# Performance work log

Measured on AMD Instinct MI355X. Metric: run time of the kernel, lower is better.

The kernel has to match this reference:

```python
import jax, jax.numpy as jnp
import numpy as np

HEADS = 4
SCALE = 8.0
LN_EPS = 1e-5
L2_EPS = 1e-12

def _l2norm(t):
    # F.normalize(dim=-1): t / max(||t||_2, eps)
    n = jnp.sqrt(jnp.sum(t * t, axis=-1, keepdims=True))
    return t / jnp.maximum(n, L2_EPS)

def setup_inputs() -> dict:
    key = jax.random.key(0)
    k1, k2, k3 = jax.random.split(key, 3)
    b, c, h, w = 16, 256, 32, 32
    inner = HEADS * 64
    x = jax.random.normal(k1, (b, c, h, w), dtype=jnp.float32)
    g = jnp.ones((1, c, 1, 1), dtype=jnp.float32)
    w_qkv = jax.random.normal(k2, (3 * inner, c), dtype=jnp.float32) * (1.0 / np.sqrt(c))
    w_out = jax.random.normal(k3, (c, inner), dtype=jnp.float32) * (1.0 / np.sqrt(inner))
    return {"x": x, "g": g, "w_qkv": w_qkv, "w_out": w_out}

def reference(x, g, w_qkv, w_out):
    b, c, H, W = x.shape
    n = H * W
    # channel LayerNorm (lucidrains style): mean/var over channel dim, learned gain g
    mean = jnp.mean(x, axis=1, keepdims=True)
    var = jnp.mean((x - mean) ** 2, axis=1, keepdims=True)  # unbiased=False
    xn = (x - mean) * jax.lax.rsqrt(var + LN_EPS) * g
    # 1x1 conv QKV == channel matmul
    qkv = jnp.einsum('bchw,oc->bohw', xn, w_qkv)  # [b, 3*inner, H, W]
    q, k, v = jnp.split(qkv, 3, axis=1)
    def to_bhnd(t):
        d = t.shape[1] // HEADS
        return t.reshape(b, HEADS, d, n).transpose(0, 1, 3, 2)  # b h n d
    q, k, v = map(to_bhnd, (q, k, v))
    q, k = _l2norm(q), _l2norm(k)
    sim = jnp.einsum('bhid,bhjd->bhij', q, k) * SCALE
    attn = jax.nn.softmax(sim, axis=-1)
    out = jnp.einsum('bhij,bhjd->bhid', attn, v)
    out = out.transpose(0, 1, 3, 2).reshape(b, -1, H, W)  # b (h d) H W
    return jnp.einsum('bchw,oc->bohw', out, w_out) + x
```

## Files before the change

kernel.cpp:

```cpp
#include <hip/hip_runtime.h>
#include <hip/hip_bf16.h>

typedef short short4v __attribute__((ext_vector_type(4)));
typedef short short8v __attribute__((ext_vector_type(8)));
typedef float float4v __attribute__((ext_vector_type(4)));
typedef __bf16 bf16x8 __attribute__((ext_vector_type(8)));

typedef __attribute__((address_space(1))) const unsigned int g_uint;
typedef __attribute__((address_space(3))) unsigned int lds_uint;

__device__ __forceinline__ unsigned short f2bf(float f) {
    union { float f; unsigned int i; } t;
    t.f = f;
    unsigned int u = t.i;
    u += 0x7fffu + ((u >> 16) & 1u);
    return (unsigned short)(u >> 16);
}

__device__ __forceinline__ short bfcast(float f) {
    __bf16 h = (__bf16)f;
    return __builtin_bit_cast(short, h);
}

__device__ __forceinline__ float fast_exp2(float x) {
    float r;
    asm("v_exp_f32 %0, %1\n\ts_nop 0" : "=v"(r) : "v"(x));
    return r;
}

__device__ __forceinline__ void gload_lds16(const unsigned short* g, unsigned short* l) {
    __builtin_amdgcn_global_load_lds((g_uint*)g, (lds_uint*)l, 16, 0, 0);
}

__device__ __forceinline__ bf16x8 frag128(const unsigned short* t, int row, int slot) {
    return *reinterpret_cast<const bf16x8*>(
        reinterpret_cast<const char*>(t) + row * 128 + (((slot ^ (row & 7)) << 4)));
}

__device__ __forceinline__ float4v mfma32(bf16x8 a, bf16x8 b, float4v c) {
    return __builtin_amdgcn_mfma_f32_16x16x32_bf16(a, b, c, 0, 0, 0);
}

__global__ __launch_bounds__(256) void prep_kernel(const float* __restrict__ wq,
                                                   const float* __restrict__ wo,
                                                   unsigned short* __restrict__ wqb,
                                                   unsigned short* __restrict__ wob) {
    int i = blockIdx.x * 256 + threadIdx.x;
    if (i < 196608) wqb[i] = f2bf(wq[i]);
    else            wob[i - 196608] = f2bf(wo[i - 196608]);
}

__global__ __launch_bounds__(256) void ln_kernel(const float* __restrict__ x,
                                                 const float* __restrict__ g,
                                                 unsigned short* __restrict__ xnT) {
    __shared__ float red[2][4][64];
    const int tid = threadIdx.x;
    const int p = tid & 63, cg = tid >> 6;
    const int b = blockIdx.y;
    const int pix = blockIdx.x * 64 + p;
    const float* xb = x + ((size_t)b << 18) + pix;

    float v[64];
    float s = 0.f, q = 0.f;
    #pragma unroll
    for (int cc = 0; cc < 64; ++cc) {
        v[cc] = xb[(cg * 64 + cc) << 10];
        s += v[cc]; q += v[cc] * v[cc];
    }
    red[0][cg][p] = s; red[1][cg][p] = q;
    __syncthreads();
    float ts = red[0][0][p] + red[0][1][p] + red[0][2][p] + red[0][3][p];
    float tq = red[1][0][p] + red[1][1][p] + red[1][2][p] + red[1][3][p];
    float mean = ts * (1.f / 256.f);
    float var  = tq * (1.f / 256.f) - mean * mean;
    float rstd = rsqrtf(var + 1e-5f);
    float bias = -mean * rstd;

    unsigned short* dst = xnT + (((size_t)b << 10) + pix) * 256 + cg * 64;
    #pragma unroll
    for (int cc = 0; cc < 64; cc += 8) {
        union { uint4 u; unsigned short s[8]; } pk;
        #pragma unroll
        for (int j = 0; j < 8; ++j)
            pk.s[j] = f2bf(fmaf(v[cc + j], rstd, bias) * g[cg * 64 + cc + j]);
        *reinterpret_cast<uint4*>(dst + cc) = pk.u;
    }
}

__global__ __launch_bounds__(256) void qkv_gemm(const unsigned short* __restrict__ xnT,
                                                const unsigned short* __restrict__ wqkv,
                                                unsigned short* __restrict__ qhat,
                                                unsigned short* __restrict__ khatT,
                                                unsigned short* __restrict__ vperm) {
    __shared__ __align__(16) unsigned short sW[8192];
    __shared__ __align__(16) unsigned short sX[8192];
    const int tid = threadIdx.x, lane = tid & 63, w = tid >> 6;
    const int l16 = lane & 15, g = lane >> 4;
    const int id = blockIdx.x;
    const int xcd = id & 7, sIdx = id >> 3;
    const int m = sIdx % 12, tq = sIdx / 12;
    const int t = xcd + (tq << 3);
    const int pb = t & 15, b = t >> 4;

    const unsigned short* Wbase = wqkv + m * 64 * 256;
    const unsigned short* Xbase = xnT + (((size_t)b << 10) + pb * 64) * 256;

    const int srow = (lane >> 3);
    const int sslot = lane & 7;

    auto stage = [&](int buf, int k0) {
        #pragma unroll
        for (int ii = 0; ii < 2; ++ii) {
            int inst = w + 4 * ii;
            int row = inst * 8 + srow;
            int src = row * 256 + k0 + 8 * (sslot ^ (row & 7));
            gload_lds16(Wbase + src, &sW[buf * 4096 + inst * 512]);
            gload_lds16(Xbase + src, &sX[buf * 4096 + inst * 512]);
        }
    };

    float4v acc[4] = {{0,0,0,0},{0,0,0,0},{0,0,0,0},{0,0,0,0}};
    const bool qk = (m < 8);

    stage(0, 0);
    __syncthreads();
    for (int ks = 0; ks < 4; ++ks) {
        if (ks < 3) stage((ks + 1) & 1, (ks + 1) * 64);
        const unsigned short* Wt = &sW[(ks & 1) * 4096];
        const unsigned short* Xt = &sX[(ks & 1) * 4096];
        #pragma unroll
        for (int kk = 0; kk < 2; ++kk) {
            bf16x8 aF = frag128(qk ? Xt : Wt, 16 * w + l16, 4 * kk + g);
            #pragma unroll
            for (int jt = 0; jt < 4; ++jt) {
                bf16x8 bF = frag128(qk ? Wt : Xt, 16 * jt + l16, 4 * kk + g);
                acc[jt] = mfma32(aF, bF, acc[jt]);
            }
        }
        __syncthreads();
    }

    if (qk) {
        float rn[4];
        #pragma unroll
        for (int r = 0; r < 4; ++r) {
            float s = acc[0][r]*acc[0][r] + acc[1][r]*acc[1][r]
                    + acc[2][r]*acc[2][r] + acc[3][r]*acc[3][r];
            s += __shfl_xor(s, 1, 64);
            s += __shfl_xor(s, 2, 64);
            s += __shfl_xor(s, 4, 64);
            s += __shfl_xor(s, 8, 64);
            rn[r] = rsqrtf(fmaxf(s, 1e-24f));
        }
        int h = m & 3;
        int bh = b * 4 + h;
        if (m < 4) {
            unsigned short* qb = qhat + ((size_t)bh << 16) + (size_t)(pb * 64 + 16 * w) * 64;
            #pragma unroll
            for (int jt = 0; jt < 4; ++jt)
                #pragma unroll
                for (int r = 0; r < 4; ++r)
                    qb[(4 * g + r) * 64 + 16 * jt + l16] =
                        f2bf(acc[jt][r] * (rn[r] * 11.541560327111707f));
        } else {
            unsigned short* kb = khatT + ((size_t)(bh * 16 + pb)) * 4096;
            #pragma unroll
            for (int jt = 0; jt < 4; ++jt)
                #pragma unroll
                for (int r = 0; r < 4; ++r) {
                    int j = 16 * w + 4 * g + r;
                    int d = 16 * jt + l16;
                    kb[j * 64 + (((d >> 3) ^ (j & 7)) << 3) + (d & 7)] =
                        f2bf(acc[jt][r] * rn[r]);
                }
        }
    } else {
        int bh = b * 4 + (m - 8);
        unsigned short* vb = vperm + ((size_t)(bh * 16 + pb)) * 4096;
        #pragma unroll
        for (int jt = 0; jt < 4; ++jt) {
            int cphi = (l16 >> 2) * 2 + (jt >> 1);
            int cplo = (jt & 1) * 4 + (l16 & 3);
            #pragma unroll
            for (int r = 0; r < 4; ++r) {
                int d = 16 * w + 4 * g + r;
                vb[d * 64 + ((cphi ^ (d & 7)) << 3) + cplo] = f2bf(acc[jt][r]);
            }
        }
    }
}

__global__ __launch_bounds__(512, 4) void attn_kernel(const unsigned short* __restrict__ qhat,
                                                      const unsigned short* __restrict__ khatT,
                                                      const unsigned short* __restrict__ vperm,
                                                      unsigned short* __restrict__ oT) {
    __shared__ __align__(16) unsigned short smem[16384];
    const int tid = threadIdx.x, lane = tid & 63, w = tid >> 6;
    const int l16 = lane & 15, g = lane >> 4;
    const int id = blockIdx.x;
    const int sIdx = id >> 3;
    const int bh = (id & 7) * 8 + (sIdx >> 3);
    const int qb = sIdx & 7;
    const int b = bh >> 2, h = bh & 3;

    const unsigned short* Qg = qhat + ((size_t)bh << 16) + (size_t)(qb * 128) * 64;
    const unsigned short* Kt = khatT + ((size_t)(bh * 16)) * 4096;
    const unsigned short* Vt = vperm + ((size_t)(bh * 16)) * 4096;

    bf16x8 bq[2];
    #pragma unroll
    for (int ds = 0; ds < 2; ++ds)
        bq[ds] = *reinterpret_cast<const bf16x8*>(
            Qg + (16 * w + l16) * 64 + 32 * ds + 8 * g);

    auto stage = [&](int buf, int t) {
        unsigned short* kb = &smem[buf * 8192 + w * 512];
        unsigned short* vb = &smem[buf * 8192 + 4096 + w * 512];
        gload_lds16(Kt + t * 4096 + w * 512 + lane * 8, kb);
        gload_lds16(Vt + t * 4096 + w * 512 + lane * 8, vb);
    };

    float lsum = 0.f;
    float4v oacc[4] = {};

    stage(0, 0);
    __syncthreads();

    for (int t = 0; t < 16; ++t) {
        const unsigned short* kb = &smem[(t & 1) * 8192];
        const unsigned short* vb = kb + 4096;
        if (t < 15) stage((t + 1) & 1, t + 1);

        float4v st[4] = {};
        #pragma unroll
        for (int ds = 0; ds < 2; ++ds) {
            bf16x8 ak[4];
            #pragma unroll
            for (int jt = 0; jt < 4; ++jt)
                ak[jt] = frag128(kb, 16 * jt + l16, 4 * ds + g);
            __builtin_amdgcn_s_setprio(1);
            #pragma unroll
            for (int jt = 0; jt < 4; ++jt)
                st[jt] = mfma32(ak[jt], bq[ds], st[jt]);
            __builtin_amdgcn_s_setprio(0);
        }

        short8v vv[4][2];
        #pragma unroll
        for (int dt = 0; dt < 4; ++dt) {
            int row = 16 * dt + l16;
            #pragma unroll
            for (int q = 0; q < 2; ++q)
                vv[dt][q] = *reinterpret_cast<const short8v*>(
                    reinterpret_cast<const char*>(vb) + row * 128 +
                    (((2 * g + q) ^ (row & 7)) << 4));
        }

        short4v pf[4];
        #pragma unroll
        for (int jt = 0; jt < 4; ++jt) {
            float p0 = fast_exp2(st[jt][0]);
            float p1 = fast_exp2(st[jt][1]);
            float p2 = fast_exp2(st[jt][2]);
            float p3 = fast_exp2(st[jt][3]);
            lsum += (p0 + p1) + (p2 + p3);
            short4v tt;
            tt[0] = bfcast(p0); tt[1] = bfcast(p1);
            tt[2] = bfcast(p2); tt[3] = bfcast(p3);
            pf[jt] = tt;
        }

        __builtin_amdgcn_s_setprio(1);
        #pragma unroll
        for (int dt = 0; dt < 4; ++dt)
            #pragma unroll
            for (int q = 0; q < 2; ++q) {
                short4v lo = __builtin_shufflevector(vv[dt][q], vv[dt][q], 0, 1, 2, 3);
                short4v hi = __builtin_shufflevector(vv[dt][q], vv[dt][q], 4, 5, 6, 7);
                oacc[dt] = __builtin_amdgcn_mfma_f32_16x16x16bf16_1k(
                    lo, pf[2 * q], oacc[dt], 0, 0, 0);
                oacc[dt] = __builtin_amdgcn_mfma_f32_16x16x16bf16_1k(
                    hi, pf[2 * q + 1], oacc[dt], 0, 0, 0);
            }
        __builtin_amdgcn_s_setprio(0);

        __syncthreads();
    }

    lsum += __shfl_xor(lsum, 16, 64);
    lsum += __shfl_xor(lsum, 32, 64);
    float inv = 1.f / lsum;

    unsigned short* OL = smem;
    {
        int irow = 16 * w + l16;
        #pragma unroll
        for (int dt = 0; dt < 4; ++dt)
            #pragma unroll
            for (int r = 0; r < 4; ++r)
                OL[irow * 72 + 16 * dt + 4 * g + r] = f2bf(oacc[dt][r] * inv);
    }
    __syncthreads();
    {
        int row = tid >> 2, q4 = tid & 3;
        unsigned short* dst = oT + (((size_t)b << 10) + qb * 128 + row) * 256 + h * 64 + q4 * 16;
        const unsigned short* src = OL + row * 72 + q4 * 16;
        *reinterpret_cast<uint4*>(dst)     = *reinterpret_cast<const uint4*>(src);
        *reinterpret_cast<uint4*>(dst + 8) = *reinterpret_cast<const uint4*>(src + 8);
    }
}

__global__ __launch_bounds__(256) void out_gemm(const unsigned short* __restrict__ oT,
                                                const unsigned short* __restrict__ wout,
                                                const float* __restrict__ x,
                                                float* __restrict__ out) {
    __shared__ __align__(16) unsigned short sW[8192];
    __shared__ __align__(16) unsigned short sX[8192];
    const int tid = threadIdx.x, lane = tid & 63, w = tid >> 6;
    const int l16 = lane & 15, g = lane >> 4;
    const int id = blockIdx.x;
    const int xcd = id & 7, sIdx = id >> 3;
    const int m = sIdx & 3, tq = sIdx >> 2;
    const int t = xcd + (tq << 3);
    const int pb = t & 15, b = t >> 4;

    const unsigned short* Wbase = wout + m * 64 * 256;
    const unsigned short* Xbase = oT + (((size_t)b << 10) + pb * 64) * 256;

    const int srow = (lane >> 3);
    const int sslot = lane & 7;

    auto stage = [&](int buf, int k0) {
        #pragma unroll
        for (int ii = 0; ii < 2; ++ii) {
            int inst = w + 4 * ii;
            int row = inst * 8 + srow;
            int src = row * 256 + k0 + 8 * (sslot ^ (row & 7));
            gload_lds16(Wbase + src, &sW[buf * 4096 + inst * 512]);
            gload_lds16(Xbase + src, &sX[buf * 4096 + inst * 512]);
        }
    };

    float4v acc[4] = {{0,0,0,0},{0,0,0,0},{0,0,0,0},{0,0,0,0}};
    stage(0, 0);
    __syncthreads();
    for (int ks = 0; ks < 4; ++ks) {
        if (ks < 3) stage((ks + 1) & 1, (ks + 1) * 64);
        const unsigned short* Wt = &sW[(ks & 1) * 4096];
        const unsigned short* Xt = &sX[(ks & 1) * 4096];
        #pragma unroll
        for (int kk = 0; kk < 2; ++kk) {
            bf16x8 aF = frag128(Wt, 16 * w + l16, 4 * kk + g);
            #pragma unroll
            for (int jt = 0; jt < 4; ++jt) {
                bf16x8 bF = frag128(Xt, 16 * jt + l16, 4 * kk + g);
                acc[jt] = mfma32(aF, bF, acc[jt]);
            }
        }
        __syncthreads();
    }

    #pragma unroll
    for (int jt = 0; jt < 4; ++jt)
        #pragma unroll
        for (int r = 0; r < 4; ++r) {
            size_t idx = ((size_t)b << 18) + (size_t)(m * 64 + 16 * w + 4 * g + r) * 1024
                       + pb * 64 + 16 * jt + l16;
            out[idx] = acc[jt][r] + x[idx];
        }
}

extern "C" void kernel_launch(void* const* d_in, const int* in_sizes, int n_in,
                              void* d_out, int out_size, void* d_ws, size_t ws_size,
                              hipStream_t stream) {
    const float* x  = (const float*)d_in[0];
    const float* g  = (const float*)d_in[1];
    const float* wq = (const float*)d_in[2];
    const float* wo = (const float*)d_in[3];
    float* out = (float*)d_out;

    char* ws = (char*)d_ws;
    unsigned short* xnT   = (unsigned short*)(ws);
    unsigned short* qhat  = (unsigned short*)(ws + 8388608);
    unsigned short* khatT = (unsigned short*)(ws + 16777216);
    unsigned short* vperm = (unsigned short*)(ws + 25165824);
    unsigned short* wqb   = (unsigned short*)(ws + 33554432);
    unsigned short* wob   = (unsigned short*)(ws + 33947648);
    unsigned short* oT    = xnT;

    prep_kernel<<<1024, 256, 0, stream>>>(wq, wo, wqb, wob);
    ln_kernel<<<dim3(16, 16), 256, 0, stream>>>(x, g, xnT);
    qkv_gemm<<<3072, 256, 0, stream>>>(xnT, wqb, qhat, khatT, vperm);
    attn_kernel<<<512, 512, 0, stream>>>(qhat, khatT, vperm, oT);
    out_gemm<<<1024, 256, 0, stream>>>(oT, wob, x, out);
}
```

Measured before the change: 68.48 us.

## Fuse channel LayerNorm into QKV GEMM and prefetch full K tiles into LDS

Removes the separate LayerNorm kernel: each QKV GEMM block now loads fp32 x for its 64 pixels, computes channel mean/variance itself, and writes normalized bf16 activations straight into swizzled LDS. Weights for all four K slices are loaded up front rather than double-buffered. The same full-K prefetch replaces the double buffer in the output GEMM. This avoids the intermediate xnT write/read and one launch, but LN work and fp32 x reads are repeated across the 12 output-channel blocks per tile, and LDS use doubles to 64 KB per block, which reduces occupancy.

```diff
diff --git a/kernel.cpp b/kernel.cpp
--- a/kernel.cpp
+++ b/kernel.cpp
@@ -50,50 +50,14 @@
     else            wob[i - 196608] = f2bf(wo[i - 196608]);
 }
 
-__global__ __launch_bounds__(256) void ln_kernel(const float* __restrict__ x,
-                                                 const float* __restrict__ g,
-                                                 unsigned short* __restrict__ xnT) {
-    __shared__ float red[2][4][64];
-    const int tid = threadIdx.x;
-    const int p = tid & 63, cg = tid >> 6;
-    const int b = blockIdx.y;
-    const int pix = blockIdx.x * 64 + p;
-    const float* xb = x + ((size_t)b << 18) + pix;
-
-    float v[64];
-    float s = 0.f, q = 0.f;
-    #pragma unroll
-    for (int cc = 0; cc < 64; ++cc) {
-        v[cc] = xb[(cg * 64 + cc) << 10];
-        s += v[cc]; q += v[cc] * v[cc];
-    }
-    red[0][cg][p] = s; red[1][cg][p] = q;
-    __syncthreads();
-    float ts = red[0][0][p] + red[0][1][p] + red[0][2][p] + red[0][3][p];
-    float tq = red[1][0][p] + red[1][1][p] + red[1][2][p] + red[1][3][p];
-    float mean = ts * (1.f / 256.f);
-    float var  = tq * (1.f / 256.f) - mean * mean;
-    float rstd = rsqrtf(var + 1e-5f);
-    float bias = -mean * rstd;
-
-    unsigned short* dst = xnT + (((size_t)b << 10) + pix) * 256 + cg * 64;
-    #pragma unroll
-    for (int cc = 0; cc < 64; cc += 8) {
-        union { uint4 u; unsigned short s[8]; } pk;
-        #pragma unroll
-        for (int j = 0; j < 8; ++j)
-            pk.s[j] = f2bf(fmaf(v[cc + j], rstd, bias) * g[cg * 64 + cc + j]);
-        *reinterpret_cast<uint4*>(dst + cc) = pk.u;
-    }
-}
-
-__global__ __launch_bounds__(256) void qkv_gemm(const unsigned short* __restrict__ xnT,
-                                                const unsigned short* __restrict__ wqkv,
-                                                unsigned short* __restrict__ qhat,
-                                                unsigned short* __restrict__ khatT,
-                                                unsigned short* __restrict__ vperm) {
-    __shared__ __align__(16) unsigned short sW[8192];
-    __shared__ __align__(16) unsigned short sX[8192];
+__global__ __launch_bounds__(256) void ln_qkv_gemm(const float* __restrict__ x,
+                                                   const float* __restrict__ gam,
+                                                   const unsigned short* __restrict__ wqkv,
+                                                   unsigned short* __restrict__ qhat,
+                                                   unsigned short* __restrict__ khatT,
+                                                   unsigned short* __restrict__ vperm) {
+    __shared__ __align__(16) unsigned short sW[16384];
+    __shared__ __align__(16) unsigned short sX[16384];
     const int tid = threadIdx.x, lane = tid & 63, w = tid >> 6;
     const int l16 = lane & 15, g = lane >> 4;
     const int id = blockIdx.x;
@@ -103,31 +67,63 @@
     const int pb = t & 15, b = t >> 4;
 
     const unsigned short* Wbase = wqkv + m * 64 * 256;
-    const unsigned short* Xbase = xnT + (((size_t)b << 10) + pb * 64) * 256;
-
-    const int srow = (lane >> 3);
-    const int sslot = lane & 7;
-
-    auto stage = [&](int buf, int k0) {
+    const int srow = lane >> 3, sslot = lane & 7;
+
+    #pragma unroll
+    for (int ks = 0; ks < 4; ++ks)
         #pragma unroll
         for (int ii = 0; ii < 2; ++ii) {
             int inst = w + 4 * ii;
             int row = inst * 8 + srow;
-            int src = row * 256 + k0 + 8 * (sslot ^ (row & 7));
-            gload_lds16(Wbase + src, &sW[buf * 4096 + inst * 512]);
-            gload_lds16(Xbase + src, &sX[buf * 4096 + inst * 512]);
-        }
-    };
+            int src = row * 256 + ks * 64 + 8 * (sslot ^ (row & 7));
+            gload_lds16(Wbase + src, &sW[ks * 4096 + inst * 512]);
+        }
+
+    float* red = (float*)sX;
+    const int p = tid & 63, cg = tid >> 6;
+    const float* xb = x + ((size_t)b << 18) + pb * 64 + p;
+
+    float v[64];
+    float s = 0.f, q = 0.f;
+    #pragma unroll
+    for (int cc = 0; cc < 64; ++cc) {
+        v[cc] = xb[(cg * 64 + cc) << 10];
+        s += v[cc]; q += v[cc] * v[cc];
+    }
+    red[(0 * 4 + cg) * 64 + p] = s;
+    red[(1 * 4 + cg) * 64 + p] = q;
+    __syncthreads();
+    float ts = 0.f, tqv = 0.f;
+    #pragma unroll
+    for (int k = 0; k < 4; ++k) {
+        ts  += red[(0 * 4 + k) * 64 + p];
+        tqv += red[(1 * 4 + k) * 64 + p];
+    }
+    float mean = ts * (1.f / 256.f);
+    float var  = tqv * (1.f / 256.f) - mean * mean;
+    float rstd = rsqrtf(var + 1e-5f);
+    float bias = -mean * rstd;
+    __syncthreads();
+
+    {
+        unsigned short* xrow = &sX[cg * 4096 + p * 64];
+        #pragma unroll
+        for (int sl = 0; sl < 8; ++sl) {
+            union { uint4 u; unsigned short h[8]; } pk;
+            #pragma unroll
+            for (int j = 0; j < 8; ++j)
+                pk.h[j] = f2bf(fmaf(v[sl * 8 + j], rstd, bias) * gam[cg * 64 + sl * 8 + j]);
+            *reinterpret_cast<uint4*>(xrow + ((sl ^ (p & 7)) << 3)) = pk.u;
+        }
+    }
+    __syncthreads();
 
     float4v acc[4] = {{0,0,0,0},{0,0,0,0},{0,0,0,0},{0,0,0,0}};
     const bool qk = (m < 8);
-
-    stage(0, 0);
-    __syncthreads();
+    #pragma unroll
     for (int ks = 0; ks < 4; ++ks) {
-        if (ks < 3) stage((ks + 1) & 1, (ks + 1) * 64);
-        const unsigned short* Wt = &sW[(ks & 1) * 4096];
-        const unsigned short* Xt = &sX[(ks & 1) * 4096];
+        const unsigned short* Wt = &sW[ks * 4096];
+        const unsigned short* Xt = &sX[ks * 4096];
         #pragma unroll
         for (int kk = 0; kk < 2; ++kk) {
             bf16x8 aF = frag128(qk ? Xt : Wt, 16 * w + l16, 4 * kk + g);
@@ -137,20 +133,19 @@
                 acc[jt] = mfma32(aF, bF, acc[jt]);
             }
         }
-        __syncthreads();
     }
 
     if (qk) {
         float rn[4];
         #pragma unroll
         for (int r = 0; r < 4; ++r) {
-            float s = acc[0][r]*acc[0][r] + acc[1][r]*acc[1][r]
-                    + acc[2][r]*acc[2][r] + acc[3][r]*acc[3][r];
-            s += __shfl_xor(s, 1, 64);
-            s += __shfl_xor(s, 2, 64);
-            s += __shfl_xor(s, 4, 64);
-            s += __shfl_xor(s, 8, 64);
-            rn[r] = rsqrtf(fmaxf(s, 1e-24f));
+            float ss = acc[0][r]*acc[0][r] + acc[1][r]*acc[1][r]
+                     + acc[2][r]*acc[2][r] + acc[3][r]*acc[3][r];
+            ss += __shfl_xor(ss, 1, 64);
+            ss += __shfl_xor(ss, 2, 64);
+            ss += __shfl_xor(ss, 4, 64);
+            ss += __shfl_xor(ss, 8, 64);
+            rn[r] = rsqrtf(fmaxf(ss, 1e-24f));
         }
         int h = m & 3;
         int bh = b * 4 + h;
@@ -314,8 +309,8 @@
                                                 const unsigned short* __restrict__ wout,
                                                 const float* __restrict__ x,
                                                 float* __restrict__ out) {
-    __shared__ __align__(16) unsigned short sW[8192];
-    __shared__ __align__(16) unsigned short sX[8192];
+    __shared__ __align__(16) unsigned short sW[16384];
+    __shared__ __align__(16) unsigned short sX[16384];
     const int tid = threadIdx.x, lane = tid & 63, w = tid >> 6;
     const int l16 = lane & 15, g = lane >> 4;
     const int id = blockIdx.x;
@@ -327,27 +322,25 @@
     const unsigned short* Wbase = wout + m * 64 * 256;
     const unsigned short* Xbase = oT + (((size_t)b << 10) + pb * 64) * 256;
 
-    const int srow = (lane >> 3);
-    const int sslot = lane & 7;
-
-    auto stage = [&](int buf, int k0) {
+    const int srow = lane >> 3, sslot = lane & 7;
+
+    #pragma unroll
+    for (int ks = 0; ks < 4; ++ks)
         #pragma unroll
         for (int ii = 0; ii < 2; ++ii) {
             int inst = w + 4 * ii;
             int row = inst * 8 + srow;
-            int src = row * 256 + k0 + 8 * (sslot ^ (row & 7));
-            gload_lds16(Wbase + src, &sW[buf * 4096 + inst * 512]);
-            gload_lds16(Xbase + src, &sX[buf * 4096 + inst * 512]);
-        }
-    };
+            int src = row * 256 + ks * 64 + 8 * (sslot ^ (row & 7));
+            gload_lds16(Wbase + src, &sW[ks * 4096 + inst * 512]);
+            gload_lds16(Xbase + src, &sX[ks * 4096 + inst * 512]);
+        }
+    __syncthreads();
 
     float4v acc[4] = {{0,0,0,0},{0,0,0,0},{0,0,0,0},{0,0,0,0}};
-    stage(0, 0);
-    __syncthreads();
+    #pragma unroll
     for (int ks = 0; ks < 4; ++ks) {
-        if (ks < 3) stage((ks + 1) & 1, (ks + 1) * 64);
-        const unsigned short* Wt = &sW[(ks & 1) * 4096];
-        const unsigned short* Xt = &sX[(ks & 1) * 4096];
+        const unsigned short* Wt = &sW[ks * 4096];
+        const unsigned short* Xt = &sX[ks * 4096];
         #pragma unroll
         for (int kk = 0; kk < 2; ++kk) {
             bf16x8 aF = frag128(Wt, 16 * w + l16, 4 * kk + g);
@@ -357,7 +350,6 @@
                 acc[jt] = mfma32(aF, bF, acc[jt]);
             }
         }
-        __syncthreads();
     }
 
     #pragma unroll
@@ -380,17 +372,15 @@
     float* out = (float*)d_out;
 
     char* ws = (char*)d_ws;
-    unsigned short* xnT   = (unsigned short*)(ws);
+    unsigned short* oT    = (unsigned short*)(ws);
     unsigned short* qhat  = (unsigned short*)(ws + 8388608);
     unsigned short* khatT = (unsigned short*)(ws + 16777216);
     unsigned short* vperm = (unsigned short*)(ws + 25165824);
     unsigned short* wqb   = (unsigned short*)(ws + 33554432);
     unsigned short* wob   = (unsigned short*)(ws + 33947648);
-    unsigned short* oT    = xnT;
 
     prep_kernel<<<1024, 256, 0, stream>>>(wq, wo, wqb, wob);
-    ln_kernel<<<dim3(16, 16), 256, 0, stream>>>(x, g, xnT);
-    qkv_gemm<<<3072, 256, 0, stream>>>(xnT, wqb, qhat, khatT, vperm);
+    ln_qkv_gemm<<<3072, 256, 0, stream>>>(x, g, wqb, qhat, khatT, vperm);
     attn_kernel<<<512, 512, 0, stream>>>(qhat, khatT, vperm, oT);
     out_gemm<<<1024, 256, 0, stream>>>(oT, wob, x, out);
 }
```

Result: slower. 75.73 us (+10.6%).
